# Performance work log

Measured on AMD Instinct MI355X. Metric: run time of the kernel, lower is better.

## Reference

```python
import jax, jax.numpy as jnp
import numpy as np

B, N, D, H = 4, 2048, 256, 4
DH = D // H          # 64
SCALE = DH ** (-0.5)
LN_EPS = 1e-5


def setup_inputs() -> dict:
    key = jax.random.key(0)
    ks = jax.random.split(key, 16)
    g = lambda k, shape, fan_in: jax.random.normal(k, shape, jnp.float32) / np.sqrt(fan_in)
    # Weights stored as [in, out] (pre-transposed vs torch Linear)
    return {
        "x0": jax.random.normal(ks[0], (B, N, D), jnp.float32),
        "x1": jax.random.normal(ks[1], (B, N, D), jnp.float32),
        "Wqk": g(ks[2], (D, D), D), "bqk": jnp.zeros((D,), jnp.float32),
        "Wv": g(ks[3], (D, D), D), "bv": jnp.zeros((D,), jnp.float32),
        "Wout": g(ks[4], (D, D), D), "bout": jnp.zeros((D,), jnp.float32),
        "Wf1": g(ks[5], (2 * D, 2 * D), 2 * D), "bf1": jnp.zeros((2 * D,), jnp.float32),
        "ln_g": jnp.ones((2 * D,), jnp.float32), "ln_b": jnp.zeros((2 * D,), jnp.float32),
        "Wf2": g(ks[6], (2 * D, D), 2 * D), "bf2": jnp.zeros((D,), jnp.float32),
    }


def _split_heads(t):
    # [B,N,D] -> [B,H,N,DH]
    b, n, _ = t.shape
    return t.reshape(b, n, H, DH).transpose(0, 2, 1, 3)


def _merge_heads(t):
    # [B,H,N,DH] -> [B,N,D]
    b, h, n, dh = t.shape
    return t.transpose(0, 2, 1, 3).reshape(b, n, h * dh)


def _layernorm(x, g, b):
    mu = jnp.mean(x, axis=-1, keepdims=True)
    var = jnp.mean(jnp.square(x - mu), axis=-1, keepdims=True)
    return (x - mu) * jax.lax.rsqrt(var + LN_EPS) * g + b


def reference(x0, x1, Wqk, bqk, Wv, bv, Wout, bout, Wf1, bf1, ln_g, ln_b, Wf2, bf2):
    qk0 = _split_heads(x0 @ Wqk + bqk)   # [B,H,N,DH]
    qk1 = _split_heads(x1 @ Wqk + bqk)
    v0 = _split_heads(x0 @ Wv + bv)
    v1 = _split_heads(x1 @ Wv + bv)

    ss = SCALE ** 0.5
    sim = jnp.einsum('bhid,bhjd->bhij', qk0 * ss, qk1 * ss)  # shared score matrix
    attn01 = jax.nn.softmax(sim, axis=-1)   # normalize over j
    attn10 = jax.nn.softmax(sim, axis=-2)   # normalize over i (== softmax(sim^T) transposed)
    m0 = jnp.einsum('bhij,bhjd->bhid', attn01, v1)
    m1 = jnp.einsum('bhji,bhjd->bhid', attn10, v0)

    m0 = _merge_heads(m0) @ Wout + bout   # [B,N,D]
    m1 = _merge_heads(m1) @ Wout + bout

    def ffn(x):
        h = x @ Wf1 + bf1                 # [B,N,2D]
        h = jax.nn.gelu(_layernorm(h, ln_g, ln_b), approximate=False)
        return h @ Wf2 + bf2              # [B,N,D]

    y0 = x0 + ffn(jnp.concatenate([x0, m0], axis=-1))
    y1 = x1 + ffn(jnp.concatenate([x1, m1], axis=-1))
    return (y0, y1)
```

## Files before the change

kernel.cpp:

```cpp
#include <hip/hip_runtime.h>
#include <hip/hip_bf16.h>
#include <math.h>

typedef __bf16 bf16;
typedef __attribute__((ext_vector_type(8))) __bf16 bf16x8;
typedef __attribute__((ext_vector_type(4))) __bf16 bf16x4;
typedef __attribute__((ext_vector_type(2))) __bf16 bf16x2;
typedef __attribute__((ext_vector_type(4))) float f32x4;
typedef __attribute__((ext_vector_type(16))) float f32x16;
typedef __attribute__((ext_vector_type(4))) unsigned u32x4;

#define MFMA(a,b,c)   __builtin_amdgcn_mfma_f32_16x16x32_bf16(a,b,c,0,0,0)
#define MFMA32(a,b,c) __builtin_amdgcn_mfma_f32_32x32x16_bf16(a,b,c,0,0,0)

static constexpr int Bb = 4, Nn = 2048, Hh = 4;
static constexpr float SS2 = 0.4246609001440095f;

__device__ __forceinline__ void lds16(const bf16* src, bf16* dst) {
  __builtin_amdgcn_global_load_lds(
      (const __attribute__((address_space(1))) void*)src,
      (__attribute__((address_space(3))) void*)dst, 16, 0, 0);
}

__device__ __forceinline__ f32x16 zero16() {
  f32x16 t;
#pragma unroll
  for (int i = 0; i < 16; ++i) t[i] = 0.f;
  return t;
}

__global__ __launch_bounds__(256) void prep_k(
    const float* Wqk, const float* Wv, const float* Wout, const float* bout,
    const float* Wf1, const float* Wf2, const float* x0, const float* x1,
    bf16* wqkv_t, bf16* wout_b, bf16* wfold_t, bf16* wf1b_t, bf16* wf2_t,
    bf16* xb0, bf16* xb1) {
  int id = blockIdx.x * 256 + threadIdx.x;
  if (id < 65536) { int k = id >> 8, n = id & 255; wqkv_t[n*256 + k] = (bf16)Wqk[id]; return; }
  id -= 65536;
  if (id < 65536) { int k = id >> 8, n = id & 255; wqkv_t[(256 + n)*256 + k] = (bf16)Wv[id]; return; }
  id -= 65536;
  if (id < 98304) {
    if (id < 65536) { wout_b[id] = (bf16)Wout[id]; }
    else { int id3 = id - 65536; int r = id3 >> 8, k = id3 & 255;
           wout_b[(256 + r)*256 + k] = (r == 0) ? (bf16)bout[k] : (bf16)0.f; }
    return; }
  id -= 98304;
  if (id < 131072) { int o = id & 511, k = id >> 9; wfold_t[o*512 + k] = (bf16)Wf1[k*512 + o]; return; }
  id -= 131072;
  if (id < 131072) { int o = id & 511, k = id >> 9; wf1b_t[o*256 + k] = (bf16)Wf1[(256 + k)*512 + o]; return; }
  id -= 131072;
  if (id < 131072) { int k = id >> 8, n = id & 255; wf2_t[n*512 + k] = (bf16)Wf2[id]; return; }
  id -= 131072;
  if (id < 1048576) {
    const float* xs = (id < 524288) ? x0 : x1;
    bf16* xd = (id < 524288) ? xb0 : xb1;
    int j = (id < 524288) ? id : id - 524288;
    f32x4 v = *reinterpret_cast<const f32x4*>(&xs[(size_t)j * 4]);
    bf16x4 o; o[0] = (bf16)v[0]; o[1] = (bf16)v[1]; o[2] = (bf16)v[2]; o[3] = (bf16)v[3];
    *reinterpret_cast<bf16x4*>(&xd[(size_t)j * 4]) = o;
  }
}

template<int MODE, int BN, int MINW, int REMAP>
__global__ __launch_bounds__(256, MINW) void gemm_k(
    const bf16* Aa0, const bf16* Aa1, const bf16* Ac0, const bf16* Ac1,
    const bf16* Wt, const float* bias,
    bf16* ob0, bf16* ob1, float* of0, float* of1,
    const float* res0, const float* res1) {
  constexpr int KD  = (MODE == 3 || MODE == 4) ? 512 : 256;
  constexpr int LDA = (MODE == 4) ? 512 : 256;
  constexpr int NKC = KD / 64;
  constexpr int NF  = BN / 32;

  int bx = blockIdx.x, by = blockIdx.y, bz = blockIdx.z;
  if constexpr (REMAP) {
    int id = blockIdx.x + 64 * (blockIdx.y + 4 * blockIdx.z);
    bx = ((id & 7) << 3) + ((id >> 3) & 7);
    by = (id >> 6) & 3;
    bz = id >> 8;
  }

  const bf16* Aa = bz ? Aa1 : Aa0;
  const bf16* Ac = bz ? Ac1 : Ac0;
  bf16*  ob = bz ? ob1 : ob0;
  float* of = bz ? of1 : of0;
  const float* res = bz ? res1 : res0;

  const int tid = threadIdx.x;
  const int lane = tid & 63;
  const int w = tid >> 6;
  const int wr = w >> 1, wc = w & 1;
  const int m0r = bx * 128;
  const int n0 = by * BN;
  const int r15 = lane & 15, g = lane >> 4, rb = r15 & 7;
  const int l3 = lane >> 3, l7 = lane & 7;
  const int swzc = (l7 ^ l3) * 8;

  __shared__ bf16 At[2][8192];
  __shared__ bf16 Bt[2][BN * 64];

  const bf16* aA = Aa + (size_t)(m0r + w*32 + l3) * LDA + swzc;
  const bf16* aC = (MODE == 3) ? (Ac + (size_t)(m0r + w*32 + l3) * 256 + swzc) : nullptr;
  const bf16* bB = Wt + (size_t)(n0 + w*(BN/4) + l3) * KD + swzc;
  const int adst = (w*32) * 64;
  const int bdst = (w*(BN/4)) * 64;

  auto stage = [&](int buf, int kc) {
    const bf16* ab; int kcol;
    if constexpr (MODE == 3) {
      if (kc < 4) { ab = aA; kcol = kc * 64; } else { ab = aC; kcol = (kc - 4) * 64; }
    } else { ab = aA; kcol = kc * 64; }
#pragma unroll
    for (int i = 0; i < 4; i++)
      lds16(ab + kcol + (size_t)i * 8 * LDA, &At[buf][adst + i*512]);
#pragma unroll
    for (int i = 0; i < NF; i++)
      lds16(bB + kc*64 + (size_t)i * 8 * KD, &Bt[buf][bdst + i*512]);
  };

  f32x4 acc[4][NF];
#pragma unroll
  for (int i = 0; i < 4; i++)
#pragma unroll
    for (int j = 0; j < NF; j++) acc[i][j] = f32x4{0.f, 0.f, 0.f, 0.f};

  const int rx0 = ((0*4 + g) ^ rb) << 4;
  const int rx1 = ((1*4 + g) ^ rb) << 4;

  auto compute = [&](int cur) {
    const char* Ap = (const char*)&At[cur][0];
    const char* Bp = (const char*)&Bt[cur][0];
    __builtin_amdgcn_s_setprio(1);
#pragma unroll
    for (int ks = 0; ks < 2; ++ks) {
      const int rx = ks ? rx1 : rx0;
      bf16x8 af[4], bfr[NF];
#pragma unroll
      for (int mf = 0; mf < 4; ++mf)
        af[mf] = *reinterpret_cast<const bf16x8*>(Ap + (wr*64 + mf*16 + r15) * 128 + rx);
#pragma unroll
      for (int nf = 0; nf < NF; ++nf)
        bfr[nf] = *reinterpret_cast<const bf16x8*>(Bp + (wc*(BN/2) + nf*16 + r15) * 128 + rx);
#pragma unroll
      for (int mf = 0; mf < 4; ++mf)
#pragma unroll
        for (int nf = 0; nf < NF; ++nf)
          acc[mf][nf] = MFMA(af[mf], bfr[nf], acc[mf][nf]);
    }
    __builtin_amdgcn_s_setprio(0);
  };

  stage(0, 0);
  int cur = 0;
  for (int kc = 0; kc < NKC - 1; ++kc) {
    stage(cur ^ 1, kc + 1);
    if constexpr (NF == 4) asm volatile("s_waitcnt vmcnt(8)" ::: "memory");
    else                   asm volatile("s_waitcnt vmcnt(6)" ::: "memory");
    __builtin_amdgcn_sched_barrier(0);
    __builtin_amdgcn_s_barrier();
    __builtin_amdgcn_sched_barrier(0);
    compute(cur);
    asm volatile("s_waitcnt lgkmcnt(0)" ::: "memory");
    __builtin_amdgcn_sched_barrier(0);
    __builtin_amdgcn_s_barrier();
    __builtin_amdgcn_sched_barrier(0);
    cur ^= 1;
  }
  asm volatile("s_waitcnt vmcnt(0)" ::: "memory");
  __builtin_amdgcn_sched_barrier(0);
  __builtin_amdgcn_s_barrier();
  __builtin_amdgcn_sched_barrier(0);
  compute(cur);

#pragma unroll
  for (int mf = 0; mf < 4; ++mf)
#pragma unroll
    for (int nf = 0; nf < NF; ++nf) {
      f32x4 c = acc[mf][nf];
      int cg = n0 + wc*(BN/2) + nf*16 + r15;
#pragma unroll
      for (int r = 0; r < 4; ++r) {
        int rg = m0r + wr*64 + mf*16 + g*4 + r;
        if constexpr (MODE == 5) {
          int b = rg >> 11, n = rg & 2047;
          if (cg < 256) {
            float val = (c[r] + bias[cg]) * SS2;
            int h = cg >> 6, dh = cg & 63;
            ob[(((size_t)(b*Hh + h)) * Nn + n) * 64 + dh] = (bf16)val;
          } else {
            int c2 = cg - 256;
            float val = c[r] + res[c2];
            int h = c2 >> 6, dh = c2 & 63;
            ((bf16*)of)[(((size_t)(b*Hh + h)) * 64 + dh) * Nn + n] = (bf16)val;
          }
        } else if constexpr (MODE == 6) {
          if (rg < 256) ob[(size_t)cg * 512 + 256 + rg] = (bf16)c[r];
          else if (rg == 256) of[cg] = c[r] + bias[cg];
        } else if constexpr (MODE == 3) {
          ob[(size_t)rg * 512 + cg] = (bf16)(c[r] + bias[cg]);
        } else {
          of[(size_t)rg * 256 + cg] = c[r] + bias[cg] + (float)Ac[(size_t)rg * 256 + cg];
        }
      }
    }
}

__global__ __launch_bounds__(256, 2) void attn_k(
    const bf16* qks0, const bf16* qks1, const bf16* vT0, const bf16* vT1,
    bf16* m0o, bf16* m1o) {
  const int B = blockIdx.x + 16 * (blockIdx.y + 16 * blockIdx.z);
  const int xcd = B & 7, kk = B >> 3;
  const int group = 4 * xcd + (kk >> 4);
  const int it = kk & 15;
  const int bh = group & 15, dir = group >> 4;

  const bf16* Q  = (dir ? qks1 : qks0) + (size_t)bh * (Nn * 64);
  const bf16* Kp = (dir ? qks0 : qks1) + (size_t)bh * (Nn * 64);
  const bf16* Vp = (dir ? vT0  : vT1 ) + (size_t)bh * (64 * Nn);
  bf16* out = dir ? m1o : m0o;
  const int b = bh >> 2, h = bh & 3;

  const int tid = threadIdx.x, lane = tid & 63, w = tid >> 6;
  const int l31 = lane & 31, hi = lane >> 5, xr = l31 & 7;
  const int iw = it * 128 + w * 32;

  __shared__ bf16 Kt[2][4096];
  __shared__ bf16 Vt[2][4096];

  bf16x8 qf[4];
#pragma unroll
  for (int kt = 0; kt < 4; ++kt)
    qf[kt] = *reinterpret_cast<const bf16x8*>(
        &Q[(size_t)(iw + l31) * 64 + kt*16 + hi*8]);

  bf16x8 ones;
#pragma unroll
  for (int i = 0; i < 8; ++i) ones[i] = (bf16)1.0f;

  f32x16 acc[2]; acc[0] = zero16(); acc[1] = zero16();
  f32x16 rsacc = zero16();

  const int l3 = lane >> 3, l7 = lane & 7;
  const int swz = ((l7 ^ l3) * 8);
  const bf16* ks0 = Kp + (size_t)(w*16 +     l3) * 64 + swz;
  const bf16* ks1 = Kp + (size_t)(w*16 + 8 + l3) * 64 + swz;
  const bf16* vs0 = Vp + (size_t)(w*16 +     l3) * 2048 + swz;
  const bf16* vs1 = Vp + (size_t)(w*16 + 8 + l3) * 2048 + swz;
  const int kd0 = (w*16    ) * 64;
  const int kd1 = (w*16 + 8) * 64;

  auto stage = [&](int buf, int j0) {
    lds16(ks0 + (size_t)j0 * 64, &Kt[buf][kd0]);
    lds16(ks1 + (size_t)j0 * 64, &Kt[buf][kd1]);
    lds16(vs0 + j0,              &Vt[buf][kd0]);
    lds16(vs1 + j0,              &Vt[buf][kd1]);
  };

  int kby[2][4], vby[2][4];
#pragma unroll
  for (int jm = 0; jm < 2; ++jm)
#pragma unroll
    for (int kt = 0; kt < 4; ++kt)
      kby[jm][kt] = (jm*32 + l31) * 128 + (((2*kt + hi) ^ xr) << 4);
#pragma unroll
  for (int nt = 0; nt < 2; ++nt)
#pragma unroll
    for (int gg = 0; gg < 4; ++gg)
      vby[nt][gg] = (nt*32 + l31) * 128 + (((2*gg + hi) ^ xr) << 4);

  auto compute_tile = [&](int cur) {
    const char* Kb = (const char*)&Kt[cur][0];
    const char* Vb = (const char*)&Vt[cur][0];
    f32x16 st[2];
    __builtin_amdgcn_s_setprio(1);
#pragma unroll
    for (int jm = 0; jm < 2; ++jm) {
      f32x16 t = zero16();
#pragma unroll
      for (int kt = 0; kt < 4; ++kt) {
        bf16x8 kf = *reinterpret_cast<const bf16x8*>(Kb + kby[jm][kt]);
        t = MFMA32(kf, qf[kt], t);
      }
      st[jm] = t;
    }
    __builtin_amdgcn_s_setprio(0);
    bf16x8 pa[4];
#pragma unroll
    for (int jm = 0; jm < 2; ++jm) {
      unsigned dw[8];
#pragma unroll
      for (int s = 0; s < 8; ++s) {
        float e0 = __builtin_amdgcn_exp2f(st[jm][2*s]);
        float e1 = __builtin_amdgcn_exp2f(st[jm][2*s + 1]);
        asm("v_cvt_pk_bf16_f32 %0, %1, %2" : "=v"(dw[s]) : "v"(e0), "v"(e1));
      }
#pragma unroll
      for (int kt2 = 0; kt2 < 2; ++kt2) {
        unsigned a0 = dw[4*kt2 + 0], b0 = dw[4*kt2 + 2];
        unsigned a1 = dw[4*kt2 + 1], b1 = dw[4*kt2 + 3];
        asm volatile("v_permlane32_swap_b32 %0, %1" : "+v"(a0), "+v"(b0));
        asm volatile("v_permlane32_swap_b32 %0, %1" : "+v"(a1), "+v"(b1));
        u32x4 uu; uu[0] = a0; uu[1] = a1; uu[2] = b0; uu[3] = b1;
        pa[jm*2 + kt2] = __builtin_bit_cast(bf16x8, uu);
      }
    }
    __builtin_amdgcn_s_setprio(1);
#pragma unroll
    for (int gg = 0; gg < 4; ++gg) {
      rsacc = MFMA32(pa[gg], ones, rsacc);
#pragma unroll
      for (int nt = 0; nt < 2; ++nt) {
        bf16x8 vf = *reinterpret_cast<const bf16x8*>(Vb + vby[nt][gg]);
        acc[nt] = MFMA32(pa[gg], vf, acc[nt]);
      }
    }
    __builtin_amdgcn_s_setprio(0);
  };

  stage(0, 0);
  int cur = 0;
  for (int jt = 0; jt < 31; ++jt) {
    stage(cur ^ 1, (jt + 1) << 6);
    asm volatile("s_waitcnt vmcnt(4)" ::: "memory");
    __builtin_amdgcn_sched_barrier(0);
    __builtin_amdgcn_s_barrier();
    __builtin_amdgcn_sched_barrier(0);
    compute_tile(cur);
    asm volatile("s_waitcnt lgkmcnt(0)" ::: "memory");
    __builtin_amdgcn_sched_barrier(0);
    __builtin_amdgcn_s_barrier();
    __builtin_amdgcn_sched_barrier(0);
    cur ^= 1;
  }
  asm volatile("s_waitcnt vmcnt(0)" ::: "memory");
  __builtin_amdgcn_sched_barrier(0);
  __builtin_amdgcn_s_barrier();
  __builtin_amdgcn_sched_barrier(0);
  compute_tile(cur);

#pragma unroll
  for (int r = 0; r < 16; ++r) {
    float inv = 1.0f / rsacc[r];
    int row = iw + (r & 3) + 8*(r >> 2) + 4*hi;
#pragma unroll
    for (int nt = 0; nt < 2; ++nt) {
      int col = h*64 + nt*32 + l31;
      out[((size_t)b * Nn + row) * 256 + col] = (bf16)(acc[nt][r] * inv);
    }
  }
}

__global__ __launch_bounds__(256) void ln_gelu_k(
    bf16* hg, const float* g, const float* bb) {
  const int row = (blockIdx.x << 2) + (threadIdx.x >> 6);
  const int lane = threadIdx.x & 63;
  bf16* hr = hg + (size_t)row * 512 + lane * 8;
  bf16x8 v = *reinterpret_cast<const bf16x8*>(hr);
  float f[8];
  float s = 0.f, sq = 0.f;
#pragma unroll
  for (int i = 0; i < 8; ++i) { f[i] = (float)v[i]; s += f[i]; sq += f[i]*f[i]; }
#pragma unroll
  for (int m = 1; m < 64; m <<= 1) { s += __shfl_xor(s, m); sq += __shfl_xor(sq, m); }
  float mu = s * (1.f / 512.f);
  float var = sq * (1.f / 512.f) - mu * mu;
  float rsv = rsqrtf(var + 1e-5f);
  f32x4 g0 = *reinterpret_cast<const f32x4*>(&g[lane*8]);
  f32x4 g1 = *reinterpret_cast<const f32x4*>(&g[lane*8 + 4]);
  f32x4 b0 = *reinterpret_cast<const f32x4*>(&bb[lane*8]);
  f32x4 b1 = *reinterpret_cast<const f32x4*>(&bb[lane*8 + 4]);
  bf16x8 o;
#pragma unroll
  for (int i = 0; i < 8; ++i) {
    float gv = (i < 4) ? g0[i] : g1[i-4];
    float bv = (i < 4) ? b0[i] : b1[i-4];
    float xn = (f[i] - mu) * rsv * gv + bv;
    float ge = 0.5f * xn * (1.f + erff(xn * 0.70710678118f));
    o[i] = (bf16)ge;
  }
  *reinterpret_cast<bf16x8*>(hr) = o;
}

extern "C" void kernel_launch(void* const* d_in, const int* in_sizes, int n_in,
                              void* d_out, int out_size, void* d_ws, size_t ws_size,
                              hipStream_t stream) {
  (void)in_sizes; (void)n_in; (void)out_size; (void)ws_size;
  const float* x0   = (const float*)d_in[0];
  const float* x1   = (const float*)d_in[1];
  const float* Wqk  = (const float*)d_in[2];
  const float* bqk  = (const float*)d_in[3];
  const float* Wv   = (const float*)d_in[4];
  const float* bv   = (const float*)d_in[5];
  const float* Wout = (const float*)d_in[6];
  const float* bout = (const float*)d_in[7];
  const float* Wf1  = (const float*)d_in[8];
  const float* bf1  = (const float*)d_in[9];
  const float* ln_g = (const float*)d_in[10];
  const float* ln_b = (const float*)d_in[11];
  const float* Wf2  = (const float*)d_in[12];
  const float* bf2  = (const float*)d_in[13];
  float* y = (float*)d_out;

  bf16* p = (bf16*)d_ws;
  bf16* wqkv_t = p; p += 131072;
  bf16* wout_b = p; p += 98304;
  bf16* wfold_t = p; p += 262144;
  bf16* wf1b_t = p; p += 131072;
  bf16* wf2_t  = p; p += 131072;
  float* bfold = (float*)p; p += 1024;
  bf16* xb0  = p; p += 2097152;
  bf16* xb1  = p; p += 2097152;
  bf16* qks0 = p; p += 2097152;
  bf16* qks1 = p; p += 2097152;
  bf16* vT0  = p; p += 2097152;
  bf16* vT1  = p; p += 2097152;
  bf16* m0   = p; p += 2097152;
  bf16* m1   = p; p += 2097152;
  bf16* hg0  = p; p += 4194304;
  bf16* hg1  = p; p += 4194304;

  dim3 blk(256);
  prep_k<<<6528, blk, 0, stream>>>(Wqk, Wv, Wout, bout, Wf1, Wf2, x0, x1,
                                   wqkv_t, wout_b, wfold_t, wf1b_t, wf2_t, xb0, xb1);
  gemm_k<6,128,2,0><<<dim3(3, 4, 1), blk, 0, stream>>>(
      wout_b, wout_b, nullptr, nullptr, wf1b_t, bf1,
      wfold_t, wfold_t, bfold, bfold, nullptr, nullptr);
  gemm_k<5,128,2,1><<<dim3(64, 4, 2), blk, 0, stream>>>(
      xb0, xb1, nullptr, nullptr, wqkv_t, bqk,
      qks0, qks1, (float*)vT0, (float*)vT1, bv, bv);
  attn_k<<<dim3(16, 16, 2), blk, 0, stream>>>(qks0, qks1, vT0, vT1, m0, m1);
  gemm_k<3,128,2,1><<<dim3(64, 4, 2), blk, 0, stream>>>(
      xb0, xb1, m0, m1, wfold_t, bfold,
      hg0, hg1, nullptr, nullptr, nullptr, nullptr);
  ln_gelu_k<<<dim3(4096), blk, 0, stream>>>(hg0, ln_g, ln_b);
  gemm_k<4,64,3,1><<<dim3(64, 4, 2), blk, 0, stream>>>(
      hg0, hg1, xb0, xb1, wf2_t, bf2,
      nullptr, nullptr, y, y + 2097152, nullptr, nullptr);
}
```

Baseline: 129.8 us.

## Double query rows per wave in attention and sum row totals with VALU

Each wave now handles 64 query rows instead of 32, in two 32-row halves that share every K/V fragment read from LDS. The grid is halved to 256 blocks and launch bounds drop to one block per SIMD slot. The ones-matrix MFMA for row sums is replaced by scalar adds of the exponentials, reduced across half-waves with a shuffle and passed through a small LDS table for the final normalisation. This cuts LDS traffic and MFMA work per score element, but raises register pressure and gives fewer blocks to hide latency.

```diff
diff --git a/kernel.cpp b/kernel.cpp
--- a/kernel.cpp
+++ b/kernel.cpp
@@ -205,13 +205,13 @@
     }
 }
 
-__global__ __launch_bounds__(256, 2) void attn_k(
+__global__ __launch_bounds__(256, 1) void attn_k(
     const bf16* qks0, const bf16* qks1, const bf16* vT0, const bf16* vT1,
     bf16* m0o, bf16* m1o) {
-  const int B = blockIdx.x + 16 * (blockIdx.y + 16 * blockIdx.z);
+  const int B = blockIdx.x + 8 * (blockIdx.y + 16 * blockIdx.z);
   const int xcd = B & 7, kk = B >> 3;
-  const int group = 4 * xcd + (kk >> 4);
-  const int it = kk & 15;
+  const int group = 4 * xcd + (kk >> 3);
+  const int it = kk & 7;
   const int bh = group & 15, dir = group >> 4;
 
   const bf16* Q  = (dir ? qks1 : qks0) + (size_t)bh * (Nn * 64);
@@ -222,23 +222,26 @@
 
   const int tid = threadIdx.x, lane = tid & 63, w = tid >> 6;
   const int l31 = lane & 31, hi = lane >> 5, xr = l31 & 7;
-  const int iw = it * 128 + w * 32;
+  const int iw = it * 256 + w * 64;
 
   __shared__ bf16 Kt[2][4096];
   __shared__ bf16 Vt[2][4096];
-
-  bf16x8 qf[4];
-#pragma unroll
-  for (int kt = 0; kt < 4; ++kt)
-    qf[kt] = *reinterpret_cast<const bf16x8*>(
-        &Q[(size_t)(iw + l31) * 64 + kt*16 + hi*8]);
-
-  bf16x8 ones;
-#pragma unroll
-  for (int i = 0; i < 8; ++i) ones[i] = (bf16)1.0f;
-
-  f32x16 acc[2]; acc[0] = zero16(); acc[1] = zero16();
-  f32x16 rsacc = zero16();
+  __shared__ float Rt[4][64];
+
+  bf16x8 qf[2][4];
+#pragma unroll
+  for (int ih = 0; ih < 2; ++ih)
+#pragma unroll
+    for (int kt = 0; kt < 4; ++kt)
+      qf[ih][kt] = *reinterpret_cast<const bf16x8*>(
+          &Q[(size_t)(iw + ih*32 + l31) * 64 + kt*16 + hi*8]);
+
+  f32x16 acc[2][2];
+#pragma unroll
+  for (int ih = 0; ih < 2; ++ih)
+#pragma unroll
+    for (int nt = 0; nt < 2; ++nt) acc[ih][nt] = zero16();
+  float rsum0 = 0.f, rsum1 = 0.f;
 
   const int l3 = lane >> 3, l7 = lane & 7;
   const int swz = ((l7 ^ l3) * 8);
@@ -271,48 +274,49 @@
   auto compute_tile = [&](int cur) {
     const char* Kb = (const char*)&Kt[cur][0];
     const char* Vb = (const char*)&Vt[cur][0];
-    f32x16 st[2];
-    __builtin_amdgcn_s_setprio(1);
+    bf16x8 pa[2][4];
 #pragma unroll
     for (int jm = 0; jm < 2; ++jm) {
-      f32x16 t = zero16();
+      f32x16 st0 = zero16(), st1 = zero16();
+      __builtin_amdgcn_s_setprio(1);
 #pragma unroll
       for (int kt = 0; kt < 4; ++kt) {
         bf16x8 kf = *reinterpret_cast<const bf16x8*>(Kb + kby[jm][kt]);
-        t = MFMA32(kf, qf[kt], t);
+        st0 = MFMA32(kf, qf[0][kt], st0);
+        st1 = MFMA32(kf, qf[1][kt], st1);
       }
-      st[jm] = t;
-    }
-    __builtin_amdgcn_s_setprio(0);
-    bf16x8 pa[4];
-#pragma unroll
-    for (int jm = 0; jm < 2; ++jm) {
-      unsigned dw[8];
-#pragma unroll
-      for (int s = 0; s < 8; ++s) {
-        float e0 = __builtin_amdgcn_exp2f(st[jm][2*s]);
-        float e1 = __builtin_amdgcn_exp2f(st[jm][2*s + 1]);
-        asm("v_cvt_pk_bf16_f32 %0, %1, %2" : "=v"(dw[s]) : "v"(e0), "v"(e1));
-      }
-#pragma unroll
-      for (int kt2 = 0; kt2 < 2; ++kt2) {
-        unsigned a0 = dw[4*kt2 + 0], b0 = dw[4*kt2 + 2];
-        unsigned a1 = dw[4*kt2 + 1], b1 = dw[4*kt2 + 3];
-        asm volatile("v_permlane32_swap_b32 %0, %1" : "+v"(a0), "+v"(b0));
-        asm volatile("v_permlane32_swap_b32 %0, %1" : "+v"(a1), "+v"(b1));
-        u32x4 uu; uu[0] = a0; uu[1] = a1; uu[2] = b0; uu[3] = b1;
-        pa[jm*2 + kt2] = __builtin_bit_cast(bf16x8, uu);
+      __builtin_amdgcn_s_setprio(0);
+#pragma unroll
+      for (int ih = 0; ih < 2; ++ih) {
+        const f32x16& st = ih ? st1 : st0;
+        unsigned dw[8];
+#pragma unroll
+        for (int s = 0; s < 8; ++s) {
+          float e0 = __builtin_amdgcn_exp2f(st[2*s]);
+          float e1 = __builtin_amdgcn_exp2f(st[2*s + 1]);
+          if (ih) rsum1 += e0 + e1; else rsum0 += e0 + e1;
+          asm("v_cvt_pk_bf16_f32 %0, %1, %2" : "=v"(dw[s]) : "v"(e0), "v"(e1));
+        }
+#pragma unroll
+        for (int kt2 = 0; kt2 < 2; ++kt2) {
+          unsigned a0 = dw[4*kt2 + 0], b0 = dw[4*kt2 + 2];
+          unsigned a1 = dw[4*kt2 + 1], b1 = dw[4*kt2 + 3];
+          asm volatile("v_permlane32_swap_b32 %0, %1" : "+v"(a0), "+v"(b0));
+          asm volatile("v_permlane32_swap_b32 %0, %1" : "+v"(a1), "+v"(b1));
+          u32x4 uu; uu[0] = a0; uu[1] = a1; uu[2] = b0; uu[3] = b1;
+          pa[ih][jm*2 + kt2] = __builtin_bit_cast(bf16x8, uu);
+        }
       }
     }
     __builtin_amdgcn_s_setprio(1);
 #pragma unroll
     for (int gg = 0; gg < 4; ++gg) {
-      rsacc = MFMA32(pa[gg], ones, rsacc);
-#pragma unroll
-      for (int nt = 0; nt < 2; ++nt) {
-        bf16x8 vf = *reinterpret_cast<const bf16x8*>(Vb + vby[nt][gg]);
-        acc[nt] = MFMA32(pa[gg], vf, acc[nt]);
-      }
+      bf16x8 v0 = *reinterpret_cast<const bf16x8*>(Vb + vby[0][gg]);
+      bf16x8 v1 = *reinterpret_cast<const bf16x8*>(Vb + vby[1][gg]);
+      acc[0][0] = MFMA32(pa[0][gg], v0, acc[0][0]);
+      acc[1][0] = MFMA32(pa[1][gg], v0, acc[1][0]);
+      acc[0][1] = MFMA32(pa[0][gg], v1, acc[0][1]);
+      acc[1][1] = MFMA32(pa[1][gg], v1, acc[1][1]);
     }
     __builtin_amdgcn_s_setprio(0);
   };
@@ -338,16 +342,30 @@
   __builtin_amdgcn_sched_barrier(0);
   compute_tile(cur);
 
-#pragma unroll
-  for (int r = 0; r < 16; ++r) {
-    float inv = 1.0f / rsacc[r];
-    int row = iw + (r & 3) + 8*(r >> 2) + 4*hi;
-#pragma unroll
-    for (int nt = 0; nt < 2; ++nt) {
-      int col = h*64 + nt*32 + l31;
-      out[((size_t)b * Nn + row) * 256 + col] = (bf16)(acc[nt][r] * inv);
+  rsum0 += __shfl_xor(rsum0, 32);
+  rsum1 += __shfl_xor(rsum1, 32);
+  if (hi == 0) {
+    Rt[w][l31]      = rsum0;
+    Rt[w][32 + l31] = rsum1;
+  }
+  f32x4 rv[2][4];
+#pragma unroll
+  for (int ih = 0; ih < 2; ++ih)
+#pragma unroll
+    for (int q = 0; q < 4; ++q)
+      rv[ih][q] = *reinterpret_cast<const f32x4*>(&Rt[w][ih*32 + 8*q + 4*hi]);
+#pragma unroll
+  for (int ih = 0; ih < 2; ++ih)
+#pragma unroll
+    for (int r = 0; r < 16; ++r) {
+      float inv = 1.0f / rv[ih][r >> 2][r & 3];
+      int row = iw + ih*32 + (r & 3) + 8*(r >> 2) + 4*hi;
+#pragma unroll
+      for (int nt = 0; nt < 2; ++nt) {
+        int col = h*64 + nt*32 + l31;
+        out[((size_t)b * Nn + row) * 256 + col] = (bf16)(acc[ih][nt][r] * inv);
+      }
     }
-  }
 }
 
 __global__ __launch_bounds__(256) void ln_gelu_k(
@@ -428,7 +446,7 @@
   gemm_k<5,128,2,1><<<dim3(64, 4, 2), blk, 0, stream>>>(
       xb0, xb1, nullptr, nullptr, wqkv_t, bqk,
       qks0, qks1, (float*)vT0, (float*)vT1, bv, bv);
-  attn_k<<<dim3(16, 16, 2), blk, 0, stream>>>(qks0, qks1, vT0, vT1, m0, m1);
+  attn_k<<<dim3(8, 16, 2), blk, 0, stream>>>(qks0, qks1, vT0, vT1, m0, m1);
   gemm_k<3,128,2,1><<<dim3(64, 4, 2), blk, 0, stream>>>(
       xb0, xb1, m0, m1, wfold_t, bfold,
       hg0, hg1, nullptr, nullptr, nullptr, nullptr);
```

Result: slower. 143.6 us (+10.6%).

## Split attention key range across two wave groups with LDS merge

Applied to the files above, without the earlier changes.

The attention kernel now runs 512 threads per block. Two groups of four waves each take half of the key/value sequence (16 tiles instead of 32), each with its own double-buffered K/V staging area in a 64KB shared buffer. At the end, the second group writes its partial output and row-sum accumulators to LDS and the first group adds them, normalizes and stores. This halves the serial loop length per wave and doubles resident waves, to better hide latency. The trade-offs are double the LDS per block, a final cross-wave reduction, and a tight register budget from launch_bounds(512,4), which may cause spills.

```diff
diff --git a/kernel.cpp b/kernel.cpp
--- a/kernel.cpp
+++ b/kernel.cpp
@@ -205,7 +205,7 @@
     }
 }
 
-__global__ __launch_bounds__(256, 2) void attn_k(
+__global__ __launch_bounds__(512, 4) void attn_k(
     const bf16* qks0, const bf16* qks1, const bf16* vT0, const bf16* vT1,
     bf16* m0o, bf16* m1o) {
   const int B = blockIdx.x + 16 * (blockIdx.y + 16 * blockIdx.z);
@@ -221,11 +221,14 @@
   const int b = bh >> 2, h = bh & 3;
 
   const int tid = threadIdx.x, lane = tid & 63, w = tid >> 6;
+  const int ig = w >> 1, hj = w & 1;
   const int l31 = lane & 31, hi = lane >> 5, xr = l31 & 7;
-  const int iw = it * 128 + w * 32;
-
-  __shared__ bf16 Kt[2][4096];
-  __shared__ bf16 Vt[2][4096];
+  const int iw = it * 128 + ig * 32;
+
+  __shared__ char smem[65536];
+  bf16* KV = (bf16*)smem;
+  const int kbase = hj * 8192;
+  const int vbase = 16384 + hj * 8192;
 
   bf16x8 qf[4];
 #pragma unroll
@@ -242,18 +245,18 @@
 
   const int l3 = lane >> 3, l7 = lane & 7;
   const int swz = ((l7 ^ l3) * 8);
-  const bf16* ks0 = Kp + (size_t)(w*16 +     l3) * 64 + swz;
-  const bf16* ks1 = Kp + (size_t)(w*16 + 8 + l3) * 64 + swz;
-  const bf16* vs0 = Vp + (size_t)(w*16 +     l3) * 2048 + swz;
-  const bf16* vs1 = Vp + (size_t)(w*16 + 8 + l3) * 2048 + swz;
-  const int kd0 = (w*16    ) * 64;
-  const int kd1 = (w*16 + 8) * 64;
+  const bf16* ks0 = Kp + (size_t)(ig*16 +     l3) * 64 + swz;
+  const bf16* ks1 = Kp + (size_t)(ig*16 + 8 + l3) * 64 + swz;
+  const bf16* vs0 = Vp + (size_t)(ig*16 +     l3) * 2048 + swz;
+  const bf16* vs1 = Vp + (size_t)(ig*16 + 8 + l3) * 2048 + swz;
+  const int kd0 = (ig*16    ) * 64;
+  const int kd1 = (ig*16 + 8) * 64;
 
   auto stage = [&](int buf, int j0) {
-    lds16(ks0 + (size_t)j0 * 64, &Kt[buf][kd0]);
-    lds16(ks1 + (size_t)j0 * 64, &Kt[buf][kd1]);
-    lds16(vs0 + j0,              &Vt[buf][kd0]);
-    lds16(vs1 + j0,              &Vt[buf][kd1]);
+    lds16(ks0 + (size_t)j0 * 64, KV + kbase + buf*4096 + kd0);
+    lds16(ks1 + (size_t)j0 * 64, KV + kbase + buf*4096 + kd1);
+    lds16(vs0 + j0,              KV + vbase + buf*4096 + kd0);
+    lds16(vs1 + j0,              KV + vbase + buf*4096 + kd1);
   };
 
   int kby[2][4], vby[2][4];
@@ -269,8 +272,8 @@
       vby[nt][gg] = (nt*32 + l31) * 128 + (((2*gg + hi) ^ xr) << 4);
 
   auto compute_tile = [&](int cur) {
-    const char* Kb = (const char*)&Kt[cur][0];
-    const char* Vb = (const char*)&Vt[cur][0];
+    const char* Kb = (const char*)(KV + kbase + cur*4096);
+    const char* Vb = (const char*)(KV + vbase + cur*4096);
     f32x16 st[2];
     __builtin_amdgcn_s_setprio(1);
 #pragma unroll
@@ -317,10 +320,11 @@
     __builtin_amdgcn_s_setprio(0);
   };
 
-  stage(0, 0);
+  const int jt0 = hj << 4;
+  stage(0, jt0 << 6);
   int cur = 0;
-  for (int jt = 0; jt < 31; ++jt) {
-    stage(cur ^ 1, (jt + 1) << 6);
+  for (int t = 0; t < 15; ++t) {
+    stage(cur ^ 1, (jt0 + t + 1) << 6);
     asm volatile("s_waitcnt vmcnt(4)" ::: "memory");
     __builtin_amdgcn_sched_barrier(0);
     __builtin_amdgcn_s_barrier();
@@ -338,14 +342,31 @@
   __builtin_amdgcn_sched_barrier(0);
   compute_tile(cur);
 
-#pragma unroll
-  for (int r = 0; r < 16; ++r) {
-    float inv = 1.0f / rsacc[r];
-    int row = iw + (r & 3) + 8*(r >> 2) + 4*hi;
-#pragma unroll
-    for (int nt = 0; nt < 2; ++nt) {
-      int col = h*64 + nt*32 + l31;
-      out[((size_t)b * Nn + row) * 256 + col] = (bf16)(acc[nt][r] * inv);
+  __syncthreads();
+  float* Ex = (float*)smem;
+  if (hj == 1) {
+#pragma unroll
+    for (int nt = 0; nt < 2; ++nt)
+#pragma unroll
+      for (int r = 0; r < 16; ++r)
+        Ex[(ig*48 + nt*16 + r) * 64 + lane] = acc[nt][r];
+#pragma unroll
+    for (int r = 0; r < 16; ++r)
+      Ex[(ig*48 + 32 + r) * 64 + lane] = rsacc[r];
+  }
+  __syncthreads();
+  if (hj == 0) {
+#pragma unroll
+    for (int r = 0; r < 16; ++r) {
+      float rs = rsacc[r] + Ex[(ig*48 + 32 + r) * 64 + lane];
+      float inv = 1.0f / rs;
+      int row = iw + (r & 3) + 8*(r >> 2) + 4*hi;
+#pragma unroll
+      for (int nt = 0; nt < 2; ++nt) {
+        float o = acc[nt][r] + Ex[(ig*48 + nt*16 + r) * 64 + lane];
+        int col = h*64 + nt*32 + l31;
+        out[((size_t)b * Nn + row) * 256 + col] = (bf16)(o * inv);
+      }
     }
   }
 }
@@ -428,7 +449,7 @@
   gemm_k<5,128,2,1><<<dim3(64, 4, 2), blk, 0, stream>>>(
       xb0, xb1, nullptr, nullptr, wqkv_t, bqk,
       qks0, qks1, (float*)vT0, (float*)vT1, bv, bv);
-  attn_k<<<dim3(16, 16, 2), blk, 0, stream>>>(qks0, qks1, vT0, vT1, m0, m1);
+  attn_k<<<dim3(16, 16, 2), dim3(512), 0, stream>>>(qks0, qks1, vT0, vT1, m0, m1);
   gemm_k<3,128,2,1><<<dim3(64, 4, 2), blk, 0, stream>>>(
       xb0, xb1, m0, m1, wfold_t, bfold,
       hg0, hg1, nullptr, nullptr, nullptr, nullptr);
```

Result: no change. 129.4 us (-0.3%).
